# Performance work log

Measured on AMD Instinct MI355X. Metric: run time of the kernel, lower is better.

Reference implementation:

```python
import jax, jax.numpy as jnp
import numpy as np

N_HEADS = 16

def setup_inputs() -> dict:
    key = jax.random.key(0)
    ks = jax.random.split(key, 9)
    B, L, D = 4, 2048, 1024
    s = D ** -0.5
    return {
        "x": jax.random.normal(ks[0], (B, L, D), dtype=jnp.float32),
        "Wq": jax.random.normal(ks[1], (D, D), dtype=jnp.float32) * s,
        "bq": jax.random.normal(ks[2], (D,), dtype=jnp.float32) * 0.02,
        "Wk": jax.random.normal(ks[3], (D, D), dtype=jnp.float32) * s,
        "bk": jax.random.normal(ks[4], (D,), dtype=jnp.float32) * 0.02,
        "Wv": jax.random.normal(ks[5], (D, D), dtype=jnp.float32) * s,
        "bv": jax.random.normal(ks[6], (D,), dtype=jnp.float32) * 0.02,
        "Wo": jax.random.normal(ks[7], (D, D), dtype=jnp.float32) * s,
        "bo": jax.random.normal(ks[8], (D,), dtype=jnp.float32) * 0.02,
    }

def reference(x, Wq, bq, Wk, bk, Wv, bv, Wo, bo):
    B, L, D = x.shape
    H = N_HEADS
    hd = D // H
    scale = hd ** -0.5
    # torch Linear: y = x @ W.T + b
    q = (x @ Wq.T + bq).reshape(B, L, H, hd)
    k = (x @ Wk.T + bk).reshape(B, L, H, hd)
    v = (x @ Wv.T + bv).reshape(B, L, H, hd)
    # scores [B,H,L,L]
    qk = jnp.einsum('bqhd,bkhd->bhqk', q, k) * scale
    causal = jnp.tril(jnp.ones((L, L), dtype=bool))
    qk = jnp.where(causal[None, None, :, :], qk, -jnp.inf)
    attn = jax.nn.softmax(qk, axis=-1)
    out = jnp.einsum('bhqk,bkhd->bqhd', attn, v).reshape(B, L, D)
    return out @ Wo.T + bo
```

## Files before the change

kernel.cpp:

```cpp
#include <hip/hip_runtime.h>
#include <hip/hip_bf16.h>
#include <math.h>

#define Bsz 4
#define Lsz 2048
#define Dsz 1024
#define Hn 16
#define HDsz 64
#define NQT 16

typedef __attribute__((ext_vector_type(8))) short short8;
typedef __attribute__((ext_vector_type(4))) float floatx4;
typedef unsigned short ushort_t;

__device__ __forceinline__ void load_lds_16B(const void* g, void* l) {
    __builtin_amdgcn_global_load_lds(
        (const __attribute__((address_space(1))) unsigned int*)g,
        (__attribute__((address_space(3))) unsigned int*)l, 16, 0, 0);
}

__device__ inline void cvt_store(float* p, size_t i, float v) { p[i] = v; }
__device__ inline void cvt_store(__hip_bfloat16* p, size_t i, float v) {
    p[i] = __float2bfloat16(v);
}

__device__ inline ushort_t f2bf_raw(float f) {
    __hip_bfloat16 b = __float2bfloat16(f);
    return *reinterpret_cast<ushort_t*>(&b);
}

__device__ inline float bf2f_raw(ushort_t u) {
    union { unsigned int i; float f; } c;
    c.i = ((unsigned int)u) << 16;
    return c.f;
}

__device__ __forceinline__ float fast_exp2(float x) {
#if __has_builtin(__builtin_amdgcn_exp2f)
    return __builtin_amdgcn_exp2f(x);
#else
    return exp2f(x);
#endif
}

__device__ __forceinline__ unsigned pk_bf16_rhu(float p0, float p1) {
    return __builtin_amdgcn_perm(__builtin_bit_cast(unsigned, p1) + 0x8000u,
                                 __builtin_bit_cast(unsigned, p0) + 0x8000u,
                                 0x07060302u);
}

__global__ __launch_bounds__(256) void f2b(const float* __restrict__ in,
                                           __hip_bfloat16* __restrict__ out,
                                           int n) {
    int i = (blockIdx.x * 256 + threadIdx.x) * 4;
    if (i >= n) return;
    float4 v = *(const float4*)(in + i);
    out[i + 0] = __float2bfloat16(v.x);
    out[i + 1] = __float2bfloat16(v.y);
    out[i + 2] = __float2bfloat16(v.z);
    out[i + 3] = __float2bfloat16(v.w);
}

__global__ __launch_bounds__(256) void f2b4(const float* __restrict__ w0,
                                            const float* __restrict__ w1,
                                            const float* __restrict__ w2,
                                            const float* __restrict__ w3,
                                            __hip_bfloat16* __restrict__ out) {
    int bid = blockIdx.x;
    int sel = bid >> 10;
    const float* in = sel == 0 ? w0 : (sel == 1 ? w1 : (sel == 2 ? w2 : w3));
    size_t off = (size_t)(bid & 1023) * 1024 + threadIdx.x * 4;
    float4 v = *(const float4*)(in + off);
    __hip_bfloat16* o = out + (size_t)sel * (1024 * 1024) + off;
    o[0] = __float2bfloat16(v.x);
    o[1] = __float2bfloat16(v.y);
    o[2] = __float2bfloat16(v.z);
    o[3] = __float2bfloat16(v.w);
}

template <typename TO, bool QKV>
__global__ __launch_bounds__(512, 2) void gemm_bt_256(
    const ushort_t* __restrict__ A, const ushort_t* __restrict__ W,
    const float* __restrict__ b0, const float* __restrict__ b1,
    const float* __restrict__ b2, TO* __restrict__ C, int M, int N, int K) {
    __shared__ ushort_t As[2][256 * 64];
    __shared__ ushort_t Bs[2][256 * 64];

    const int t = threadIdx.x;
    const int wave = t >> 6, lane = t & 63;
    const int lmod = lane & 15, quad = lane >> 4;
    const int wm = wave >> 2, wn = wave & 3;

    const int nbn = N >> 8;
    const int nwg = nbn * (M >> 8);
    const int bid = blockIdx.x;
    const int wg = (bid & 7) * (nwg >> 3) + (bid >> 3);
    const int n0 = (wg % nbn) * 256, m0 = (wg / nbn) * 256;

    floatx4 acc[2][2][4][2] = {};
    short8 Af[4][2], Bf[2][2];

    const int NT = K >> 6;

    auto stageA = [&](int kt, int bi) {
        const int kk = kt << 6;
#pragma unroll
        for (int p = 0; p < 4; p++) {
            int slot = t + p * 512;
            int row = slot >> 3, c8 = slot & 7;
            int gc8 = c8 ^ (row & 7);
            load_lds_16B(A + (size_t)(m0 + row) * K + kk + gc8 * 8,
                         &As[bi][slot * 8]);
        }
    };
    auto stageB = [&](int kt, int bi) {
        const int kk = kt << 6;
#pragma unroll
        for (int p = 0; p < 4; p++) {
            int slot = t + p * 512;
            int row = slot >> 3, c8 = slot & 7;
            int gc8 = c8 ^ (row & 7);
            load_lds_16B(W + (size_t)(n0 + row) * K + kk + gc8 * 8,
                         &Bs[bi][slot * 8]);
        }
    };
    auto rdA = [&](int bi, int mh) {
#pragma unroll
        for (int mr = 0; mr < 4; mr++) {
            int row = wm * 128 + mh * 64 + mr * 16 + lmod;
#pragma unroll
            for (int ks = 0; ks < 2; ks++) {
                int sc8 = (ks * 4 + quad) ^ (row & 7);
                Af[mr][ks] = *(const short8*)&As[bi][row * 64 + sc8 * 8];
            }
        }
    };
    auto rdB = [&](int bi, int nh) {
#pragma unroll
        for (int nr = 0; nr < 2; nr++) {
            int row = wn * 64 + nh * 32 + nr * 16 + lmod;
#pragma unroll
            for (int ks = 0; ks < 2; ks++) {
                int sc8 = (ks * 4 + quad) ^ (row & 7);
                Bf[nr][ks] = *(const short8*)&Bs[bi][row * 64 + sc8 * 8];
            }
        }
    };
    auto domm = [&](int mh, int nh) {
        __builtin_amdgcn_s_setprio(1);
#pragma unroll
        for (int mr = 0; mr < 4; mr++)
#pragma unroll
            for (int nr = 0; nr < 2; nr++)
#pragma unroll
                for (int ks = 0; ks < 2; ks++)
                    acc[mh][nh][mr][nr] =
                        __builtin_amdgcn_mfma_f32_16x16x32_bf16(
                            Af[mr][ks], Bf[nr][ks], acc[mh][nh][mr][nr], 0, 0,
                            0);
        __builtin_amdgcn_s_setprio(0);
    };

    stageA(0, 0);
    stageB(0, 0);
    asm volatile("s_waitcnt vmcnt(0)" ::: "memory");
    __builtin_amdgcn_s_barrier();
    asm volatile("" ::: "memory");

#pragma unroll 1
    for (int T = 0; T < NT; T++) {
        const int cur = T & 1, nxt = cur ^ 1;
        const bool pf = (T + 1 < NT);
        rdA(cur, 0);
        rdB(cur, 0);
        if (pf) stageA(T + 1, nxt);
        __builtin_amdgcn_s_barrier();
        __builtin_amdgcn_sched_barrier(0);
        domm(0, 0);
        __builtin_amdgcn_s_barrier();
        rdB(cur, 1);
        if (pf) stageB(T + 1, nxt);
        __builtin_amdgcn_s_barrier();
        __builtin_amdgcn_sched_barrier(0);
        domm(0, 1);
        __builtin_amdgcn_s_barrier();
        rdA(cur, 1);
        __builtin_amdgcn_s_barrier();
        __builtin_amdgcn_sched_barrier(0);
        domm(1, 1);
        __builtin_amdgcn_s_barrier();
        rdB(cur, 0);
        __builtin_amdgcn_s_barrier();
        __builtin_amdgcn_sched_barrier(0);
        domm(1, 0);
        asm volatile("s_waitcnt vmcnt(0)" ::: "memory");
        __builtin_amdgcn_s_barrier();
        asm volatile("" ::: "memory");
    }

    const int sec = QKV ? (n0 >> 10) : 0;
    const float* bp = QKV ? (sec == 0 ? b0 : (sec == 1 ? b1 : b2)) : b0;
    TO* Cb = QKV ? (C + (size_t)sec * M * 1024) : C;
    const int Nout = QKV ? 1024 : N;
    const float sc = (QKV && sec == 0) ? 0.1803368801111204f : 1.0f;

#pragma unroll
    for (int mh = 0; mh < 2; mh++)
#pragma unroll
        for (int mr = 0; mr < 4; mr++) {
            int gm = m0 + wm * 128 + mh * 64 + mr * 16 + quad * 4;
#pragma unroll
            for (int nh = 0; nh < 2; nh++)
#pragma unroll
                for (int nr = 0; nr < 2; nr++) {
                    int gn = n0 + wn * 64 + nh * 32 + nr * 16 + lmod;
                    int cn = QKV ? (gn & 1023) : gn;
                    float b = bp[cn];
#pragma unroll
                    for (int r = 0; r < 4; r++)
                        cvt_store(Cb, (size_t)(gm + r) * Nout + cn,
                                  (acc[mh][nh][mr][nr][r] + b) * sc);
                }
        }
}

template <typename TO, bool QKV>
__global__ __launch_bounds__(256) void gemm_bt_mfma(
    const ushort_t* __restrict__ A, const ushort_t* __restrict__ W,
    const float* __restrict__ b0, const float* __restrict__ b1,
    const float* __restrict__ b2, TO* __restrict__ C, int M, int N, int K) {
    __shared__ ushort_t As[128 * 32];
    __shared__ ushort_t Bs[128 * 32];

    const int t = threadIdx.x;
    const int wave = t >> 6, lane = t & 63;

    const int nbx = N >> 7;
    const int nwg = nbx * (M >> 7);
    const int bid = blockIdx.x;
    const int wg = (bid & 7) * (nwg >> 3) + (bid >> 3);
    const int n0 = (wg % nbx) * 128, m0 = (wg / nbx) * 128;

    const int wm = (wave & 1) * 64, wn = (wave >> 1) * 64;
    const int lmod = lane & 15, quad = lane >> 4;

    floatx4 acc[4][4] = {};

    for (int k0 = 0; k0 < K; k0 += 32) {
#pragma unroll
        for (int p = 0; p < 2; p++) {
            int chunk = t + p * 256;
            int r = chunk >> 2;
            int c8 = (chunk & 3) * 8;
            load_lds_16B(A + (size_t)(m0 + r) * K + k0 + c8, &As[chunk * 8]);
            load_lds_16B(W + (size_t)(n0 + r) * K + k0 + c8, &Bs[chunk * 8]);
        }
        __syncthreads();

        short8 af[4], bf_[4];
#pragma unroll
        for (int i = 0; i < 4; i++) {
            af[i] = *(const short8*)&As[(wm + i * 16 + lmod) * 32 + quad * 8];
            bf_[i] = *(const short8*)&Bs[(wn + i * 16 + lmod) * 32 + quad * 8];
        }
#pragma unroll
        for (int i = 0; i < 4; i++)
#pragma unroll
            for (int j = 0; j < 4; j++)
                acc[i][j] = __builtin_amdgcn_mfma_f32_16x16x32_bf16(
                    af[i], bf_[j], acc[i][j], 0, 0, 0);
        __syncthreads();
    }

    const int sec = n0 >> 10;
    const float* bp = QKV ? (sec == 0 ? b0 : (sec == 1 ? b1 : b2)) : b0;
    TO* Cb = QKV ? (C + (size_t)sec * M * 1024) : C;
    const int Nout = QKV ? 1024 : N;
    const float sc = (QKV && sec == 0) ? 0.1803368801111204f : 1.0f;

#pragma unroll
    for (int i = 0; i < 4; i++) {
        int gm = m0 + wm + i * 16 + quad * 4;
#pragma unroll
        for (int j = 0; j < 4; j++) {
            int gn = n0 + wn + j * 16 + lmod;
            int cn = QKV ? (gn & 1023) : gn;
            float b = bp[cn];
#pragma unroll
            for (int r = 0; r < 4; r++)
                cvt_store(Cb, (size_t)(gm + r) * Nout + cn,
                          (acc[i][j][r] + b) * sc);
        }
    }
}

__global__ __launch_bounds__(256) void attn_mfma(
    const ushort_t* __restrict__ q, const ushort_t* __restrict__ k,
    const ushort_t* __restrict__ v, ushort_t* __restrict__ Opart,
    float* __restrict__ lpart) {
    __shared__ ushort_t Ks[2][64 * 64];
    __shared__ ushort_t Vts[64 * 64];
    __shared__ ushort_t Ps[4][32 * 64];

    const int t = threadIdx.x;
    const int wave = t >> 6, lane = t & 63;
    const int lmod = lane & 15, quad = lane >> 4;

    const int bid = blockIdx.x;
    const int j = bid >> 3;
    const int bx = j & 15;
    const int p = bx & 7, s = bx >> 3;
    const int bh = (bid & 7) + ((j >> 4) << 3);
    const int b = bh >> 4, h = bh & 15;
    const size_t base = ((size_t)b * Lsz) * Dsz + h * HDsz;

    const int vrp = t & 31, vcg = t >> 5;
    ushort_t* Pw = (ushort_t*)Ps[wave];
    const int lm7 = lmod & 7;

    auto stageK = [&](int kt, int bi) {
#pragma unroll
        for (int pp = 0; pp < 2; pp++) {
            int slot = t + pp * 256;
            int row = slot >> 3, c8 = slot & 7;
            int gc8 = c8 ^ (row & 7);
            load_lds_16B(k + base + (size_t)(kt * 64 + row) * Dsz + gc8 * 8,
                         &Ks[bi][slot * 8]);
        }
    };
    auto loadV = [&](int kt, uint4& r0, uint4& r1) {
        const ushort_t* v0p =
            v + base + (size_t)(kt * 64 + 2 * vrp) * Dsz + vcg * 8;
        r0 = *(const uint4*)v0p;
        r1 = *(const uint4*)(v0p + Dsz);
    };
    auto writeV = [&](uint4 r0, uint4 r1) {
        unsigned vv0[4] = {r0.x, r0.y, r0.z, r0.w};
        unsigned vv1[4] = {r1.x, r1.y, r1.z, r1.w};
        const int kk = 2 * vrp;
        const int kc8 = kk >> 3, klo = kk & 7;
#pragma unroll
        for (int jj = 0; jj < 4; jj++) {
            int d0 = vcg * 8 + 2 * jj;
            unsigned lo = __builtin_amdgcn_perm(vv1[jj], vv0[jj], 0x05040100u);
            unsigned hi = __builtin_amdgcn_perm(vv1[jj], vv0[jj], 0x07060302u);
            *(unsigned*)&Vts[d0 * 64 + (kc8 ^ (d0 & 7)) * 8 + klo] = lo;
            int d1 = d0 + 1;
            *(unsigned*)&Vts[d1 * 64 + (kc8 ^ (d1 & 7)) * 8 + klo] = hi;
        }
    };

    int bi = 0;
    uint4 vr0, vr1;

    {
        const int kt00 = s * (NQT - p);
        stageK(kt00, 0);
        loadV(kt00, vr0, vr1);
    }

#pragma unroll 1
    for (int seg = 0; seg < 2; seg++) {
        const int qtile = seg == 0 ? (NQT - 1 - p) : p;
        const int q0 = qtile * 128;
        const int Th = qtile + 1;
        const int kt0 = s * Th, kt1 = kt0 + Th;
        const int kt0n = s * (p + 1);

        short8 aq[2][2];
#pragma unroll
        for (int g = 0; g < 2; g++) {
            const ushort_t* qp = q + base +
                                 (size_t)(q0 + wave * 32 + g * 16 + lmod) * Dsz +
                                 quad * 8;
            aq[g][0] = *(const short8*)(qp);
            aq[g][1] = *(const short8*)(qp + 32);
        }

        floatx4 Oacc[2][4] = {};
        float lsum[2] = {0.f, 0.f};

#pragma unroll 1
        for (int kt = kt0; kt < kt1; kt++) {
            asm volatile("s_waitcnt vmcnt(0)" ::: "memory");
            __builtin_amdgcn_s_barrier();
            asm volatile("" ::: "memory");

            writeV(vr0, vr1);
            asm volatile("s_waitcnt lgkmcnt(0)" ::: "memory");
            __builtin_amdgcn_s_barrier();
            asm volatile("" ::: "memory");

            const int ktn = (kt + 1 < kt1) ? kt + 1 : (seg == 0 ? kt0n : -1);
            if (ktn >= 0) stageK(ktn, bi ^ 1);

            floatx4 St[2][4] = {};
#pragma unroll
            for (int nt = 0; nt < 4; nt++) {
                int key = nt * 16 + lmod;
#pragma unroll
                for (int ks = 0; ks < 2; ks++) {
                    int sc8 = (ks * 4 + quad) ^ (key & 7);
                    short8 kf = *(const short8*)&Ks[bi][(key * 8 + sc8) * 8];
#pragma unroll
                    for (int g = 0; g < 2; g++)
                        St[g][nt] = __builtin_amdgcn_mfma_f32_16x16x32_bf16(
                            kf, aq[g][ks], St[g][nt], 0, 0, 0);
                }
            }

            const bool need_mask = (kt >= 2 * qtile);
#pragma unroll
            for (int g = 0; g < 2; g++) {
                int qg = q0 + wave * 32 + g * 16 + lmod;
#pragma unroll
                for (int nt = 0; nt < 4; nt++) {
                    int k0g = kt * 64 + nt * 16 + quad * 4;
                    float p0 = fast_exp2(St[g][nt][0]);
                    float p1 = fast_exp2(St[g][nt][1]);
                    float p2 = fast_exp2(St[g][nt][2]);
                    float p3 = fast_exp2(St[g][nt][3]);
                    if (need_mask) {
                        if (k0g + 0 > qg) p0 = 0.f;
                        if (k0g + 1 > qg) p1 = 0.f;
                        if (k0g + 2 > qg) p2 = 0.f;
                        if (k0g + 3 > qg) p3 = 0.f;
                    }
                    lsum[g] += ((p0 + p1) + (p2 + p3));
                    uint2 w;
                    w.x = pk_bf16_rhu(p0, p1);
                    w.y = pk_bf16_rhu(p2, p3);
                    int c8 = nt * 2 + (quad >> 1);
                    int sc8 = c8 ^ lm7;
                    *(uint2*)&Pw[((g * 16 + lmod) * 8 + sc8) * 8 +
                                 (quad & 1) * 4] = w;
                }
            }

            if (ktn >= 0) loadV(ktn, vr0, vr1);

            short8 ap[2][2];
#pragma unroll
            for (int g = 0; g < 2; g++)
#pragma unroll
                for (int ks = 0; ks < 2; ks++) {
                    int sc8 = (ks * 4 + quad) ^ lm7;
                    ap[g][ks] =
                        *(const short8*)&Pw[((g * 16 + lmod) * 8 + sc8) * 8];
                }
#pragma unroll
            for (int on = 0; on < 4; on++) {
                int d = on * 16 + lmod;
#pragma unroll
                for (int ks = 0; ks < 2; ks++) {
                    int sc8 = (ks * 4 + quad) ^ (d & 7);
                    short8 bv = *(const short8*)&Vts[(d * 8 + sc8) * 8];
#pragma unroll
                    for (int g = 0; g < 2; g++)
                        Oacc[g][on] = __builtin_amdgcn_mfma_f32_16x16x32_bf16(
                            ap[g][ks], bv, Oacc[g][on], 0, 0, 0);
                }
            }

            bi ^= 1;
        }

#pragma unroll
        for (int g = 0; g < 2; g++) {
            lsum[g] += __shfl_xor(lsum[g], 16);
            lsum[g] += __shfl_xor(lsum[g], 32);
        }

        const size_t rec = ((size_t)bh * NQT + qtile) * 2 + s;
        ushort_t* Orec = Opart + rec * (128 * 64);
        float* lrec = lpart + rec * 128;
#pragma unroll
        for (int g = 0; g < 2; g++) {
            if (quad == 0) lrec[wave * 32 + g * 16 + lmod] = lsum[g];
#pragma unroll
            for (int r = 0; r < 4; r++) {
                int row = wave * 32 + g * 16 + quad * 4 + r;
#pragma unroll
                for (int on = 0; on < 4; on++) {
                    int d = on * 16 + lmod;
                    Orec[row * 64 + d] = f2bf_raw(Oacc[g][on][r]);
                }
            }
        }
    }
}

__global__ __launch_bounds__(256) void attn_combine(
    const ushort_t* __restrict__ Opart, const float* __restrict__ lpart,
    ushort_t* __restrict__ ao) {
    int gidx = blockIdx.x * 256 + threadIdx.x;
    int rowglob = gidx >> 3;
    int c8 = (gidx & 7) * 8;
    int bh = rowglob >> 11;
    int r11 = rowglob & 2047;
    int qtile = r11 >> 7, row = r11 & 127;

    size_t rec0 = ((size_t)bh * NQT + qtile) * 2;
    const ushort_t* O0 = Opart + (rec0 + 0) * (128 * 64) + row * 64 + c8;
    const ushort_t* O1 = Opart + (rec0 + 1) * (128 * 64) + row * 64 + c8;
    float l = lpart[(rec0 + 0) * 128 + row] + lpart[(rec0 + 1) * 128 + row];
    float inv = 1.0f / l;

    short8 a = *(const short8*)O0;
    short8 bvec = *(const short8*)O1;
    short8 o;
#pragma unroll
    for (int j = 0; j < 8; j++) {
        float vv = (bf2f_raw((ushort_t)a[j]) + bf2f_raw((ushort_t)bvec[j])) * inv;
        o[j] = (short)f2bf_raw(vv);
    }
    int b = bh >> 4, h = bh & 15;
    int qg = qtile * 128 + row;
    *(short8*)&ao[((size_t)(b * Lsz + qg)) * Dsz + h * HDsz + c8] = o;
}

extern "C" void kernel_launch(void* const* d_in, const int* in_sizes, int n_in,
                              void* d_out, int out_size, void* d_ws,
                              size_t ws_size, hipStream_t stream) {
    const size_t elems = (size_t)Bsz * Lsz * Dsz;
    const size_t welem = (size_t)Dsz * Dsz;
    const size_t nrec = (size_t)Bsz * Hn * NQT * 2;
    const size_t opart_e = nrec * 128 * 64;
    const size_t need = (5 * elems + 4 * welem + opart_e) * 2 + nrec * 128 * 4;
    if (ws_size < need) return;

    const float* x = (const float*)d_in[0];
    const float* Wq = (const float*)d_in[1];
    const float* bq = (const float*)d_in[2];
    const float* Wk = (const float*)d_in[3];
    const float* bk = (const float*)d_in[4];
    const float* Wv = (const float*)d_in[5];
    const float* bv = (const float*)d_in[6];
    const float* Wo = (const float*)d_in[7];
    const float* bo = (const float*)d_in[8];
    float* out = (float*)d_out;

    __hip_bfloat16* xb = (__hip_bfloat16*)d_ws;
    __hip_bfloat16* q = xb + elems;
    __hip_bfloat16* k = q + elems;
    __hip_bfloat16* v = k + elems;
    __hip_bfloat16* ao = v + elems;
    __hip_bfloat16* Wqb = ao + elems;
    __hip_bfloat16* Wkb = Wqb + welem;
    __hip_bfloat16* Wvb = Wkb + welem;
    __hip_bfloat16* Wob = Wvb + welem;
    ushort_t* Opart = (ushort_t*)(Wob + welem);
    float* lpart = (float*)(Opart + opart_e);

    const int M = Bsz * Lsz, N = Dsz, K = Dsz;

    f2b<<<(int)(elems / 4 + 255) / 256, 256, 0, stream>>>(x, xb, (int)elems);
    f2b4<<<4096, 256, 0, stream>>>(Wq, Wk, Wv, Wo, Wqb);

    gemm_bt_256<__hip_bfloat16, true><<<(3 * N / 256) * (M / 256), 512, 0,
                                        stream>>>(
        (const ushort_t*)xb, (const ushort_t*)Wqb, bq, bk, bv, q, M, 3 * N, K);

    attn_mfma<<<16 * Bsz * Hn, 256, 0, stream>>>(
        (const ushort_t*)q, (const ushort_t*)k, (const ushort_t*)v, Opart,
        lpart);

    attn_combine<<<(int)(elems / 8 / 256), 256, 0, stream>>>(Opart, lpart,
                                                             (ushort_t*)ao);

    gemm_bt_mfma<float, false><<<N / 128 * (M / 128), 256, 0, stream>>>(
        (const ushort_t*)ao, (const ushort_t*)Wob, bo, bo, bo, out, M, N, K);
}
```

Baseline: 282.2 us.

## Replace output projection GEMM with 256x128 double-buffered swizzled MFMA kernel

The output projection GEMM moves from a simple 128x128, K=32 single-buffered kernel to a 256x128 tile with 8 waves, a K=64 step, XOR-swizzled LDS, double buffering and interleaved LDS reads and MFMA phases. The goal is to overlap global loads with compute and raise data reuse per tile. The QKV GEMM loop also issues the B-tile prefetch together with the A-tile prefetch at the start of each iteration. The larger tiles give fewer workgroups (256) for the output GEMM, which may limit occupancy on a large CU count.

```diff
diff --git a/kernel.cpp b/kernel.cpp
--- a/kernel.cpp
+++ b/kernel.cpp
@@ -173,13 +173,15 @@
         const bool pf = (T + 1 < NT);
         rdA(cur, 0);
         rdB(cur, 0);
-        if (pf) stageA(T + 1, nxt);
+        if (pf) {
+            stageA(T + 1, nxt);
+            stageB(T + 1, nxt);
+        }
         __builtin_amdgcn_s_barrier();
         __builtin_amdgcn_sched_barrier(0);
         domm(0, 0);
         __builtin_amdgcn_s_barrier();
         rdB(cur, 1);
-        if (pf) stageB(T + 1, nxt);
         __builtin_amdgcn_s_barrier();
         __builtin_amdgcn_sched_barrier(0);
         domm(0, 1);
@@ -224,74 +226,133 @@
         }
 }
 
-template <typename TO, bool QKV>
-__global__ __launch_bounds__(256) void gemm_bt_mfma(
+__global__ __launch_bounds__(512, 2) void gemm_out_256(
     const ushort_t* __restrict__ A, const ushort_t* __restrict__ W,
-    const float* __restrict__ b0, const float* __restrict__ b1,
-    const float* __restrict__ b2, TO* __restrict__ C, int M, int N, int K) {
-    __shared__ ushort_t As[128 * 32];
-    __shared__ ushort_t Bs[128 * 32];
+    const float* __restrict__ bo, float* __restrict__ C, int M, int N, int K) {
+    __shared__ ushort_t As[2][256 * 64];
+    __shared__ ushort_t Bs[2][128 * 64];
 
     const int t = threadIdx.x;
     const int wave = t >> 6, lane = t & 63;
-
-    const int nbx = N >> 7;
-    const int nwg = nbx * (M >> 7);
+    const int lmod = lane & 15, quad = lane >> 4;
+    const int wm = wave >> 2, wn = wave & 3;
+
+    const int nbn = N >> 7;
+    const int nwg = nbn * (M >> 8);
     const int bid = blockIdx.x;
     const int wg = (bid & 7) * (nwg >> 3) + (bid >> 3);
-    const int n0 = (wg % nbx) * 128, m0 = (wg / nbx) * 128;
-
-    const int wm = (wave & 1) * 64, wn = (wave >> 1) * 64;
-    const int lmod = lane & 15, quad = lane >> 4;
-
-    floatx4 acc[4][4] = {};
-
-    for (int k0 = 0; k0 < K; k0 += 32) {
+    const int n0 = (wg % nbn) * 128, m0 = (wg / nbn) * 256;
+
+    floatx4 acc[2][2][4] = {};
+    short8 Af[4][2], Bf[2];
+
+    const int NT = K >> 6;
+
+    auto stageA = [&](int kt, int bi) {
+        const int kk = kt << 6;
+#pragma unroll
+        for (int p = 0; p < 4; p++) {
+            int slot = t + p * 512;
+            int row = slot >> 3, c8 = slot & 7;
+            int gc8 = c8 ^ (row & 7);
+            load_lds_16B(A + (size_t)(m0 + row) * K + kk + gc8 * 8,
+                         &As[bi][slot * 8]);
+        }
+    };
+    auto stageB = [&](int kt, int bi) {
+        const int kk = kt << 6;
 #pragma unroll
         for (int p = 0; p < 2; p++) {
-            int chunk = t + p * 256;
-            int r = chunk >> 2;
-            int c8 = (chunk & 3) * 8;
-            load_lds_16B(A + (size_t)(m0 + r) * K + k0 + c8, &As[chunk * 8]);
-            load_lds_16B(W + (size_t)(n0 + r) * K + k0 + c8, &Bs[chunk * 8]);
-        }
-        __syncthreads();
-
-        short8 af[4], bf_[4];
-#pragma unroll
-        for (int i = 0; i < 4; i++) {
-            af[i] = *(const short8*)&As[(wm + i * 16 + lmod) * 32 + quad * 8];
-            bf_[i] = *(const short8*)&Bs[(wn + i * 16 + lmod) * 32 + quad * 8];
-        }
-#pragma unroll
-        for (int i = 0; i < 4; i++)
-#pragma unroll
-            for (int j = 0; j < 4; j++)
-                acc[i][j] = __builtin_amdgcn_mfma_f32_16x16x32_bf16(
-                    af[i], bf_[j], acc[i][j], 0, 0, 0);
-        __syncthreads();
+            int slot = t + p * 512;
+            int row = slot >> 3, c8 = slot & 7;
+            int gc8 = c8 ^ (row & 7);
+            load_lds_16B(W + (size_t)(n0 + row) * K + kk + gc8 * 8,
+                         &Bs[bi][slot * 8]);
+        }
+    };
+    auto rdA = [&](int bi, int mh) {
+#pragma unroll
+        for (int mr = 0; mr < 4; mr++) {
+            int row = wm * 128 + mh * 64 + mr * 16 + lmod;
+#pragma unroll
+            for (int ks = 0; ks < 2; ks++) {
+                int sc8 = (ks * 4 + quad) ^ (row & 7);
+                Af[mr][ks] = *(const short8*)&As[bi][row * 64 + sc8 * 8];
+            }
+        }
+    };
+    auto rdB = [&](int bi, int nh) {
+        int row = wn * 32 + nh * 16 + lmod;
+#pragma unroll
+        for (int ks = 0; ks < 2; ks++) {
+            int sc8 = (ks * 4 + quad) ^ (row & 7);
+            Bf[ks] = *(const short8*)&Bs[bi][row * 64 + sc8 * 8];
+        }
+    };
+    auto domm = [&](int mh, int nh) {
+        __builtin_amdgcn_s_setprio(1);
+#pragma unroll
+        for (int mr = 0; mr < 4; mr++)
+#pragma unroll
+            for (int ks = 0; ks < 2; ks++)
+                acc[mh][nh][mr] = __builtin_amdgcn_mfma_f32_16x16x32_bf16(
+                    Af[mr][ks], Bf[ks], acc[mh][nh][mr], 0, 0, 0);
+        __builtin_amdgcn_s_setprio(0);
+    };
+
+    stageA(0, 0);
+    stageB(0, 0);
+    asm volatile("s_waitcnt vmcnt(0)" ::: "memory");
+    __builtin_amdgcn_s_barrier();
+    asm volatile("" ::: "memory");
+
+#pragma unroll 1
+    for (int T = 0; T < NT; T++) {
+        const int cur = T & 1, nxt = cur ^ 1;
+        const bool pf = (T + 1 < NT);
+        rdA(cur, 0);
+        rdB(cur, 0);
+        if (pf) {
+            stageA(T + 1, nxt);
+            stageB(T + 1, nxt);
+        }
+        __builtin_amdgcn_s_barrier();
+        __builtin_amdgcn_sched_barrier(0);
+        domm(0, 0);
+        __builtin_amdgcn_s_barrier();
+        rdB(cur, 1);
+        __builtin_amdgcn_s_barrier();
+        __builtin_amdgcn_sched_barrier(0);
+        domm(0, 1);
+        __builtin_amdgcn_s_barrier();
+        rdA(cur, 1);
+        __builtin_amdgcn_s_barrier();
+        __builtin_amdgcn_sched_barrier(0);
+        domm(1, 1);
+        __builtin_amdgcn_s_barrier();
+        rdB(cur, 0);
+        __builtin_amdgcn_s_barrier();
+        __builtin_amdgcn_sched_barrier(0);
+        domm(1, 0);
+        asm volatile("s_waitcnt vmcnt(0)" ::: "memory");
+        __builtin_amdgcn_s_barrier();
+        asm volatile("" ::: "memory");
     }
 
-    const int sec = n0 >> 10;
-    const float* bp = QKV ? (sec == 0 ? b0 : (sec == 1 ? b1 : b2)) : b0;
-    TO* Cb = QKV ? (C + (size_t)sec * M * 1024) : C;
-    const int Nout = QKV ? 1024 : N;
-    const float sc = (QKV && sec == 0) ? 0.1803368801111204f : 1.0f;
-
-#pragma unroll
-    for (int i = 0; i < 4; i++) {
-        int gm = m0 + wm + i * 16 + quad * 4;
-#pragma unroll
-        for (int j = 0; j < 4; j++) {
-            int gn = n0 + wn + j * 16 + lmod;
-            int cn = QKV ? (gn & 1023) : gn;
-            float b = bp[cn];
-#pragma unroll
-            for (int r = 0; r < 4; r++)
-                cvt_store(Cb, (size_t)(gm + r) * Nout + cn,
-                          (acc[i][j][r] + b) * sc);
-        }
-    }
+#pragma unroll
+    for (int mh = 0; mh < 2; mh++)
+#pragma unroll
+        for (int mr = 0; mr < 4; mr++) {
+            int gm = m0 + wm * 128 + mh * 64 + mr * 16 + quad * 4;
+#pragma unroll
+            for (int nh = 0; nh < 2; nh++) {
+                int gn = n0 + wn * 32 + nh * 16 + lmod;
+                float b = bo[gn];
+#pragma unroll
+                for (int r = 0; r < 4; r++)
+                    C[(size_t)(gm + r) * N + gn] = acc[mh][nh][mr][r] + b;
+            }
+        }
 }
 
 __global__ __launch_bounds__(256) void attn_mfma(
@@ -568,6 +629,6 @@
     attn_combine<<<(int)(elems / 8 / 256), 256, 0, stream>>>(Opart, lpart,
                                                              (ushort_t*)ao);
 
-    gemm_bt_mfma<float, false><<<N / 128 * (M / 128), 256, 0, stream>>>(
-        (const ushort_t*)ao, (const ushort_t*)Wob, bo, bo, bo, out, M, N, K);
-}
+    gemm_out_256<<<(N / 128) * (M / 256), 512, 0, stream>>>(
+        (const ushort_t*)ao, (const ushort_t*)Wob, bo, out, M, N, K);
+}
```

Result: no change. 284.6 us (+0.9%).

## Use 256x128 tiled GEMM for QKV and output projections, fuse conversion kernels

Applied to the files above, without the earlier changes.

Shrinks the 512-thread pipelined GEMM tile from 256x256 to 256x128, so each wave computes 128x32 instead of 128x64. The QKV projection gets twice as many workgroups, and the output projection now uses this double-buffered kernel in place of the simpler 128x128 single-buffered one. The x and weight fp32-to-bf16 conversions are merged into one launch to save a kernel launch. The smaller tile lowers register and LDS pressure and improves occupancy and wave balance, but it reuses each A tile less, adding global and LDS traffic per FLOP.

```diff
diff --git a/kernel.cpp b/kernel.cpp
--- a/kernel.cpp
+++ b/kernel.cpp
@@ -49,29 +49,27 @@
                                  0x07060302u);
 }
 
-__global__ __launch_bounds__(256) void f2b(const float* __restrict__ in,
-                                           __hip_bfloat16* __restrict__ out,
-                                           int n) {
-    int i = (blockIdx.x * 256 + threadIdx.x) * 4;
-    if (i >= n) return;
-    float4 v = *(const float4*)(in + i);
-    out[i + 0] = __float2bfloat16(v.x);
-    out[i + 1] = __float2bfloat16(v.y);
-    out[i + 2] = __float2bfloat16(v.z);
-    out[i + 3] = __float2bfloat16(v.w);
-}
-
-__global__ __launch_bounds__(256) void f2b4(const float* __restrict__ w0,
-                                            const float* __restrict__ w1,
-                                            const float* __restrict__ w2,
-                                            const float* __restrict__ w3,
-                                            __hip_bfloat16* __restrict__ out) {
+__global__ __launch_bounds__(256) void f2ball(
+    const float* __restrict__ x, const float* __restrict__ w0,
+    const float* __restrict__ w1, const float* __restrict__ w2,
+    const float* __restrict__ w3, __hip_bfloat16* __restrict__ xb,
+    __hip_bfloat16* __restrict__ wb) {
     int bid = blockIdx.x;
-    int sel = bid >> 10;
-    const float* in = sel == 0 ? w0 : (sel == 1 ? w1 : (sel == 2 ? w2 : w3));
-    size_t off = (size_t)(bid & 1023) * 1024 + threadIdx.x * 4;
+    const float* in;
+    __hip_bfloat16* o;
+    size_t off;
+    if (bid < 8192) {
+        off = (size_t)bid * 1024 + threadIdx.x * 4;
+        in = x;
+        o = xb + off;
+    } else {
+        int b2 = bid - 8192;
+        int sel = b2 >> 10;
+        in = sel == 0 ? w0 : (sel == 1 ? w1 : (sel == 2 ? w2 : w3));
+        off = (size_t)(b2 & 1023) * 1024 + threadIdx.x * 4;
+        o = wb + (size_t)sel * (1024 * 1024) + off;
+    }
     float4 v = *(const float4*)(in + off);
-    __hip_bfloat16* o = out + (size_t)sel * (1024 * 1024) + off;
     o[0] = __float2bfloat16(v.x);
     o[1] = __float2bfloat16(v.y);
     o[2] = __float2bfloat16(v.z);
@@ -84,21 +82,21 @@
     const float* __restrict__ b0, const float* __restrict__ b1,
     const float* __restrict__ b2, TO* __restrict__ C, int M, int N, int K) {
     __shared__ ushort_t As[2][256 * 64];
-    __shared__ ushort_t Bs[2][256 * 64];
+    __shared__ ushort_t Bs[2][128 * 64];
 
     const int t = threadIdx.x;
     const int wave = t >> 6, lane = t & 63;
     const int lmod = lane & 15, quad = lane >> 4;
     const int wm = wave >> 2, wn = wave & 3;
 
-    const int nbn = N >> 8;
+    const int nbn = N >> 7;
     const int nwg = nbn * (M >> 8);
     const int bid = blockIdx.x;
     const int wg = (bid & 7) * (nwg >> 3) + (bid >> 3);
-    const int n0 = (wg % nbn) * 256, m0 = (wg / nbn) * 256;
-
-    floatx4 acc[2][2][4][2] = {};
-    short8 Af[4][2], Bf[2][2];
+    const int n0 = (wg % nbn) * 128, m0 = (wg / nbn) * 256;
+
+    floatx4 acc[2][2][4] = {};
+    short8 Af[4][2], Bf[2];
 
     const int NT = K >> 6;
 
@@ -116,7 +114,7 @@
     auto stageB = [&](int kt, int bi) {
         const int kk = kt << 6;
 #pragma unroll
-        for (int p = 0; p < 4; p++) {
+        for (int p = 0; p < 2; p++) {
             int slot = t + p * 512;
             int row = slot >> 3, c8 = slot & 7;
             int gc8 = c8 ^ (row & 7);
@@ -136,14 +134,11 @@
         }
     };
     auto rdB = [&](int bi, int nh) {
-#pragma unroll
-        for (int nr = 0; nr < 2; nr++) {
-            int row = wn * 64 + nh * 32 + nr * 16 + lmod;
-#pragma unroll
-            for (int ks = 0; ks < 2; ks++) {
-                int sc8 = (ks * 4 + quad) ^ (row & 7);
-                Bf[nr][ks] = *(const short8*)&Bs[bi][row * 64 + sc8 * 8];
-            }
+        int row = wn * 32 + nh * 16 + lmod;
+#pragma unroll
+        for (int ks = 0; ks < 2; ks++) {
+            int sc8 = (ks * 4 + quad) ^ (row & 7);
+            Bf[ks] = *(const short8*)&Bs[bi][row * 64 + sc8 * 8];
         }
     };
     auto domm = [&](int mh, int nh) {
@@ -151,13 +146,9 @@
 #pragma unroll
         for (int mr = 0; mr < 4; mr++)
 #pragma unroll
-            for (int nr = 0; nr < 2; nr++)
-#pragma unroll
-                for (int ks = 0; ks < 2; ks++)
-                    acc[mh][nh][mr][nr] =
-                        __builtin_amdgcn_mfma_f32_16x16x32_bf16(
-                            Af[mr][ks], Bf[nr][ks], acc[mh][nh][mr][nr], 0, 0,
-                            0);
+            for (int ks = 0; ks < 2; ks++)
+                acc[mh][nh][mr] = __builtin_amdgcn_mfma_f32_16x16x32_bf16(
+                    Af[mr][ks], Bf[ks], acc[mh][nh][mr], 0, 0, 0);
         __builtin_amdgcn_s_setprio(0);
     };
 
@@ -210,88 +201,16 @@
         for (int mr = 0; mr < 4; mr++) {
             int gm = m0 + wm * 128 + mh * 64 + mr * 16 + quad * 4;
 #pragma unroll
-            for (int nh = 0; nh < 2; nh++)
-#pragma unroll
-                for (int nr = 0; nr < 2; nr++) {
-                    int gn = n0 + wn * 64 + nh * 32 + nr * 16 + lmod;
-                    int cn = QKV ? (gn & 1023) : gn;
-                    float b = bp[cn];
-#pragma unroll
-                    for (int r = 0; r < 4; r++)
-                        cvt_store(Cb, (size_t)(gm + r) * Nout + cn,
-                                  (acc[mh][nh][mr][nr][r] + b) * sc);
-                }
-        }
-}
-
-template <typename TO, bool QKV>
-__global__ __launch_bounds__(256) void gemm_bt_mfma(
-    const ushort_t* __restrict__ A, const ushort_t* __restrict__ W,
-    const float* __restrict__ b0, const float* __restrict__ b1,
-    const float* __restrict__ b2, TO* __restrict__ C, int M, int N, int K) {
-    __shared__ ushort_t As[128 * 32];
-    __shared__ ushort_t Bs[128 * 32];
-
-    const int t = threadIdx.x;
-    const int wave = t >> 6, lane = t & 63;
-
-    const int nbx = N >> 7;
-    const int nwg = nbx * (M >> 7);
-    const int bid = blockIdx.x;
-    const int wg = (bid & 7) * (nwg >> 3) + (bid >> 3);
-    const int n0 = (wg % nbx) * 128, m0 = (wg / nbx) * 128;
-
-    const int wm = (wave & 1) * 64, wn = (wave >> 1) * 64;
-    const int lmod = lane & 15, quad = lane >> 4;
-
-    floatx4 acc[4][4] = {};
-
-    for (int k0 = 0; k0 < K; k0 += 32) {
-#pragma unroll
-        for (int p = 0; p < 2; p++) {
-            int chunk = t + p * 256;
-            int r = chunk >> 2;
-            int c8 = (chunk & 3) * 8;
-            load_lds_16B(A + (size_t)(m0 + r) * K + k0 + c8, &As[chunk * 8]);
-            load_lds_16B(W + (size_t)(n0 + r) * K + k0 + c8, &Bs[chunk * 8]);
-        }
-        __syncthreads();
-
-        short8 af[4], bf_[4];
-#pragma unroll
-        for (int i = 0; i < 4; i++) {
-            af[i] = *(const short8*)&As[(wm + i * 16 + lmod) * 32 + quad * 8];
-            bf_[i] = *(const short8*)&Bs[(wn + i * 16 + lmod) * 32 + quad * 8];
-        }
-#pragma unroll
-        for (int i = 0; i < 4; i++)
-#pragma unroll
-            for (int j = 0; j < 4; j++)
-                acc[i][j] = __builtin_amdgcn_mfma_f32_16x16x32_bf16(
-                    af[i], bf_[j], acc[i][j], 0, 0, 0);
-        __syncthreads();
-    }
-
-    const int sec = n0 >> 10;
-    const float* bp = QKV ? (sec == 0 ? b0 : (sec == 1 ? b1 : b2)) : b0;
-    TO* Cb = QKV ? (C + (size_t)sec * M * 1024) : C;
-    const int Nout = QKV ? 1024 : N;
-    const float sc = (QKV && sec == 0) ? 0.1803368801111204f : 1.0f;
-
-#pragma unroll
-    for (int i = 0; i < 4; i++) {
-        int gm = m0 + wm + i * 16 + quad * 4;
-#pragma unroll
-        for (int j = 0; j < 4; j++) {
-            int gn = n0 + wn + j * 16 + lmod;
-            int cn = QKV ? (gn & 1023) : gn;
-            float b = bp[cn];
-#pragma unroll
-            for (int r = 0; r < 4; r++)
-                cvt_store(Cb, (size_t)(gm + r) * Nout + cn,
-                          (acc[i][j][r] + b) * sc);
-        }
-    }
+            for (int nh = 0; nh < 2; nh++) {
+                int gn = n0 + wn * 32 + nh * 16 + lmod;
+                int cn = QKV ? (gn & 1023) : gn;
+                float b = bp[cn];
+#pragma unroll
+                for (int r = 0; r < 4; r++)
+                    cvt_store(Cb, (size_t)(gm + r) * Nout + cn,
+                              (acc[mh][nh][mr][r] + b) * sc);
+            }
+        }
 }
 
 __global__ __launch_bounds__(256) void attn_mfma(
@@ -554,10 +473,9 @@
 
     const int M = Bsz * Lsz, N = Dsz, K = Dsz;
 
-    f2b<<<(int)(elems / 4 + 255) / 256, 256, 0, stream>>>(x, xb, (int)elems);
-    f2b4<<<4096, 256, 0, stream>>>(Wq, Wk, Wv, Wo, Wqb);
-
-    gemm_bt_256<__hip_bfloat16, true><<<(3 * N / 256) * (M / 256), 512, 0,
+    f2ball<<<12288, 256, 0, stream>>>(x, Wq, Wk, Wv, Wo, xb, Wqb);
+
+    gemm_bt_256<__hip_bfloat16, true><<<(3 * N / 128) * (M / 256), 512, 0,
                                         stream>>>(
         (const ushort_t*)xb, (const ushort_t*)Wqb, bq, bk, bv, q, M, 3 * N, K);
 
@@ -568,6 +486,6 @@
     attn_combine<<<(int)(elems / 8 / 256), 256, 0, stream>>>(Opart, lpart,
                                                              (ushort_t*)ao);
 
-    gemm_bt_mfma<float, false><<<N / 128 * (M / 128), 256, 0, stream>>>(
+    gemm_bt_256<float, false><<<(N / 128) * (M / 256), 512, 0, stream>>>(
         (const ushort_t*)ao, (const ushort_t*)Wob, bo, bo, bo, out, M, N, K);
 }
```

Result: no change. 279.5 us (-0.9%).
